# Performance work log

Measured on AMD Instinct MI355X. Metric: run time of the kernel, lower is better.

The kernel has to match this reference:

```python
import jax, jax.numpy as jnp
import numpy as np

N_IN = 1024
N_OUT = 1024
N_SAMPLES = 64
BATCH = 4096
SIGMA_INITIAL = 0.1
MUMAX_INITIAL = 1.0


def setup_inputs() -> dict:
    key = jax.random.key(0)
    ks = jax.random.split(key, 5)
    lsig = jnp.float32(np.log(SIGMA_INITIAL))
    return {
        "x": jax.random.normal(ks[0], (BATCH, N_IN), dtype=jnp.float32),
        "w_mu": jax.random.uniform(ks[1], (N_OUT, N_IN), dtype=jnp.float32,
                                   minval=-MUMAX_INITIAL, maxval=MUMAX_INITIAL),
        "w_lsigma": jnp.full((N_OUT, N_IN), lsig, dtype=jnp.float32),
        "b_mu": jax.random.uniform(ks[2], (N_OUT,), dtype=jnp.float32,
                                   minval=-MUMAX_INITIAL, maxval=MUMAX_INITIAL),
        "b_lsigma": jnp.full((N_OUT,), lsig, dtype=jnp.float32),
        "r1": jax.random.normal(ks[3], (N_SAMPLES, N_OUT, N_IN), dtype=jnp.float32),
        "r2": jax.random.normal(ks[4], (N_SAMPLES, N_OUT), dtype=jnp.float32),
        "N_samples": N_SAMPLES,
    }


def reference(x, w_mu, w_lsigma, b_mu, b_lsigma, r1, r2, N_samples):
    # Reparameterized weight/bias samples: (S, N_out, N_in), (S, N_out)
    w = w_mu + jnp.exp(w_lsigma) * r1
    b = b_mu + jnp.exp(b_lsigma) * r2
    # y[s, b, o] = sum_i x[b, i] * w[s, o, i] + b[s, o]
    y = jnp.einsum('bi,soi->sbo', x, w) + b[:, None, :]
    return y
```

## Files before the change

### kernel.cpp

```cpp
#include <hip/hip_runtime.h>
#include <hip/hip_bf16.h>
#include <hip/hip_fp8.h>
#include <stdint.h>
#include <type_traits>

#define NIN  1024
#define NOUT 1024
#define NB   4096

typedef float f32x4  __attribute__((ext_vector_type(4)));
typedef float f32x16 __attribute__((ext_vector_type(16)));
typedef __bf16 bf16x8 __attribute__((ext_vector_type(8)));
typedef int   i32x4 __attribute__((ext_vector_type(4)));
typedef int   i32x8 __attribute__((ext_vector_type(8)));

typedef const __attribute__((address_space(1))) unsigned int* gp1_t;
typedef __attribute__((address_space(3))) unsigned int* lp3_t;

__device__ __forceinline__ void gload16(const void* g, void* l) {
    __builtin_amdgcn_global_load_lds((gp1_t)g, (lp3_t)l, 16, 0, 0);
}

__device__ __forceinline__ unsigned short f2bf(float f) {
    __bf16 h = (__bf16)f;
    return __builtin_bit_cast(unsigned short, h);
}

__device__ __forceinline__ unsigned int pk4_fp8(float a, float b, float c, float d) {
#if __has_builtin(__builtin_amdgcn_cvt_pk_fp8_f32)
    int p = __builtin_amdgcn_cvt_pk_fp8_f32(a, b, 0, false);
    p = __builtin_amdgcn_cvt_pk_fp8_f32(c, d, p, true);
    return (unsigned int)p;
#else
    __hip_fp8_e4m3 qa(a), qb(b), qc(c), qd(d);
    return (unsigned int)qa.__x | ((unsigned int)qb.__x << 8) |
           ((unsigned int)qc.__x << 16) | ((unsigned int)qd.__x << 24);
#endif
}

#define BAR   __builtin_amdgcn_s_barrier()
#define LGK0  do { asm volatile("s_waitcnt lgkmcnt(0)" ::: "memory"); __builtin_amdgcn_sched_barrier(0); } while (0)
#define VMW8  do { asm volatile("s_waitcnt vmcnt(8)"  ::: "memory"); __builtin_amdgcn_sched_barrier(0); } while (0)
#define VMW2  do { asm volatile("s_waitcnt vmcnt(2)"  ::: "memory"); __builtin_amdgcn_sched_barrier(0); } while (0)
#define VMW0  do { asm volatile("s_waitcnt vmcnt(0)"  ::: "memory"); __builtin_amdgcn_sched_barrier(0); } while (0)

__global__ void cvt_x_both(const float* __restrict__ x, unsigned short* __restrict__ xb,
                           unsigned int* __restrict__ xf8) {
    int i = blockIdx.x * blockDim.x + threadIdx.x;
    f32x4 v = reinterpret_cast<const f32x4*>(x)[i];
    ushort4 o;
    o.x = f2bf(v.x); o.y = f2bf(v.y); o.z = f2bf(v.z); o.w = f2bf(v.w);
    reinterpret_cast<ushort4*>(xb)[i] = o;
    xf8[i] = pk4_fp8(v.x, v.y, v.z, v.w);
}

__global__ void cvt_x_kernel(const float* __restrict__ x, unsigned short* __restrict__ xb) {
    int i = blockIdx.x * blockDim.x + threadIdx.x;
    f32x4 v = reinterpret_cast<const f32x4*>(x)[i];
    ushort4 o;
    o.x = f2bf(v.x); o.y = f2bf(v.y); o.z = f2bf(v.z); o.w = f2bf(v.w);
    reinterpret_cast<ushort4*>(xb)[i] = o;
}

__global__ void cvt_r1_fp8(const float* __restrict__ wls, const float* __restrict__ r1,
                           unsigned int* __restrict__ rf8, int s0) {
    int idx = blockIdx.x * blockDim.x + threadIdx.x;
    int i4 = idx & 262143;
    int c  = idx >> 18;
    f32x4 ls = reinterpret_cast<const f32x4*>(wls)[i4];
    const f32x4* rp = reinterpret_cast<const f32x4*>(r1 + ((size_t)(s0 + c) << 20));
    f32x4 r = __builtin_nontemporal_load(rp + i4);
    rf8[idx] = pk4_fp8(__expf(ls.x) * r.x, __expf(ls.y) * r.y,
                       __expf(ls.z) * r.z, __expf(ls.w) * r.w);
}

__global__ void bias_kernel(const float* __restrict__ bmu, const float* __restrict__ bls,
                            const float* __restrict__ r2, float* __restrict__ bias, int total) {
    int i = blockIdx.x * blockDim.x + threadIdx.x;
    if (i < total) {
        int o = i & (NOUT - 1);
        bias[i] = bmu[o] + __expf(bls[o]) * r2[i];
    }
}

__launch_bounds__(512, 2)
__global__ void gemm256(const unsigned short* __restrict__ xb,
                        const unsigned short* __restrict__ wb,
                        unsigned short* __restrict__ yb, int nwg) {
    __shared__ __align__(16) char smem[131072];
    const int tid = threadIdx.x;
    const int l   = tid & 63;
    const int w   = tid >> 6;
    const int wr  = w >> 2, wc = w & 3;

    const int b   = blockIdx.x;
    const int q8  = nwg >> 3;
    const int g   = (b & 7) * q8 + (b >> 3);
    const int mi  = g & 15;
    const int ni  = g >> 4;
    const int m0  = mi * 256;
    const int n0  = ni * 256;

    const int srow = l >> 3;
    const int scol = ((l & 7) ^ srow) * 8;
    const size_t slane = (size_t)srow * NIN + scol;

    const int rowp  = (l & 15) * 128;
    const int colp0 = ((l >> 4) ^ (l & 7)) << 4;

    f32x4 acc[8][4] = {};
    bf16x8 aF[4][2], b0F[2][2], b1F[2][2];

    const unsigned short* xbase = xb + (size_t)m0 * NIN;
    const unsigned short* wbase = wb + (size_t)n0 * NIN;

    auto STAGE = [&](int buf, int kt, int q) {
        const int R = (q & 3) * 64 + w * 8;
        const unsigned short* src = ((q < 4) ? xbase : wbase)
                                    + (size_t)R * NIN + kt * 64 + slane;
        char* dst = smem + buf * 65536 + ((q >= 4) ? 32768 : 0) + R * 128;
        gload16(src, dst);
    };
    auto LDA = [&](int buf, int mh) {
        const char* base = smem + buf * 65536 + (wr * 128 + mh * 64) * 128 + rowp;
        #pragma unroll
        for (int mb = 0; mb < 4; ++mb) {
            aF[mb][0] = *(const bf16x8*)(base + mb * 2048 + colp0);
            aF[mb][1] = *(const bf16x8*)(base + mb * 2048 + (colp0 ^ 64));
        }
    };
    auto LDB = [&](bf16x8 (&bF)[2][2], int buf, int nh) {
        const char* base = smem + buf * 65536 + 32768 + (wc * 64 + nh * 32) * 128 + rowp;
        #pragma unroll
        for (int nb = 0; nb < 2; ++nb) {
            bF[nb][0] = *(const bf16x8*)(base + nb * 2048 + colp0);
            bF[nb][1] = *(const bf16x8*)(base + nb * 2048 + (colp0 ^ 64));
        }
    };
    auto MM = [&](auto MHc, auto NHc, bf16x8 (&bF)[2][2]) {
        constexpr int MH = decltype(MHc)::value;
        constexpr int NH = decltype(NHc)::value;
        __builtin_amdgcn_s_setprio(1);
        #pragma unroll
        for (int mb = 0; mb < 4; ++mb)
            #pragma unroll
            for (int nb = 0; nb < 2; ++nb)
                #pragma unroll
                for (int kk = 0; kk < 2; ++kk)
                    acc[MH * 4 + mb][NH * 2 + nb] = __builtin_amdgcn_mfma_f32_16x16x32_bf16(
                        aF[mb][kk], bF[nb][kk], acc[MH * 4 + mb][NH * 2 + nb], 0, 0, 0);
        __builtin_amdgcn_s_setprio(0);
    };

    auto C0 = std::integral_constant<int, 0>{};
    auto C1 = std::integral_constant<int, 1>{};

    auto ITER = [&](auto LASTc, int t1, int t2, int t3) {
        constexpr bool LAST = decltype(LASTc)::value;
        LDA(0, 0); LDB(b0F, 0, 0);
        STAGE(1, t1, 2); STAGE(1, t1, 3);
        BAR; LGK0; MM(C0, C0, b0F); BAR;
        LDB(b1F, 0, 1);
        STAGE(1, t1, 4); STAGE(1, t1, 5);
        BAR; LGK0; MM(C0, C1, b1F); BAR;
        LDA(0, 1);
        STAGE(1, t1, 6); STAGE(1, t1, 7);
        BAR; LGK0; MM(C1, C1, b1F); BAR;
        if constexpr (!LAST) { STAGE(0, t2, 0); STAGE(0, t2, 1); }
        BAR; MM(C1, C0, b0F);
        if constexpr (LAST) { VMW0; } else { VMW2; }
        BAR;
        LDA(1, 0); LDB(b0F, 1, 0);
        if constexpr (!LAST) { STAGE(0, t2, 2); STAGE(0, t2, 3); }
        BAR; LGK0; MM(C0, C0, b0F); BAR;
        LDB(b1F, 1, 1);
        if constexpr (!LAST) { STAGE(0, t2, 4); STAGE(0, t2, 5); }
        BAR; LGK0; MM(C0, C1, b1F); BAR;
        LDA(1, 1);
        if constexpr (!LAST) { STAGE(0, t2, 6); STAGE(0, t2, 7); }
        BAR; LGK0; MM(C1, C1, b1F); BAR;
        if constexpr (!LAST) {
            STAGE(1, t3, 0); STAGE(1, t3, 1);
            BAR; MM(C1, C0, b0F); VMW2; BAR;
        } else {
            MM(C1, C0, b0F);
        }
    };

    #pragma unroll
    for (int q = 0; q < 8; ++q) STAGE(0, 0, q);
    STAGE(1, 1, 0); STAGE(1, 1, 1);
    VMW2; BAR;

    #pragma unroll 1
    for (int i = 0; i < 7; ++i)
        ITER(std::false_type{}, 2 * i + 1, 2 * i + 2, 2 * i + 3);
    ITER(std::true_type{}, 15, 16, 17);

    const int oc = n0 + wc * 64 + (l & 15);
    #pragma unroll
    for (int mb = 0; mb < 8; ++mb) {
        #pragma unroll
        for (int i2 = 0; i2 < 4; ++i2) {
            int row = m0 + wr * 128 + mb * 16 + (l >> 4) * 4 + i2;
            unsigned short* rp = yb + (size_t)row * NOUT + oc;
            #pragma unroll
            for (int nb = 0; nb < 4; ++nb)
                rp[nb * 16] = f2bf(acc[mb][nb][i2]);
        }
    }
}

__launch_bounds__(512, 2)
__global__ void gemm256mx(const unsigned char* __restrict__ xf8,
                          const unsigned char* __restrict__ rf8,
                          const unsigned short* __restrict__ y0b,
                          const float* __restrict__ bias,
                          float* __restrict__ out, int s0, int nwg) {
    __shared__ __align__(16) char smem[131072];
    const int tid = threadIdx.x;
    const int l   = tid & 63;
    const int w   = tid >> 6;
    const int wr  = w >> 2, wc = w & 3;

    const int b   = blockIdx.x;
    const int q8  = nwg >> 3;
    const int g   = (b & 7) * q8 + (b >> 3);
    const int nni = nwg >> 4;
    const int mi  = g / nni;
    const int ni  = g - mi * nni;
    const int m0  = mi * 256;
    const int n0  = ni * 256;

    const int srow  = l >> 3;
    const int scolb = ((l & 7) ^ srow) * 16;
    const size_t slane = (size_t)srow * NIN + scolb;

    const int arow = l & 31;
    const int swz  = l & 7;
    const int kgrp = (l >> 5) * 2;

    f32x16 acc[4][2] = {};
    i32x8 aF[2][2], b0F[2], b1F[2];

    const unsigned char* xbase = xf8 + (size_t)m0 * NIN;
    const unsigned char* rbase = rf8 + (size_t)n0 * NIN;

    auto STAGE = [&](int buf, int kt, int q) {
        const int R = (q & 3) * 64 + w * 8;
        const unsigned char* src = ((q < 4) ? xbase : rbase)
                                   + (size_t)R * NIN + kt * 128 + slane;
        char* dst = smem + buf * 65536 + ((q >= 4) ? 32768 : 0) + R * 128;
        gload16(src, dst);
    };
    auto STAGE8 = [&](int buf, int kt) {
        #pragma unroll
        for (int q = 0; q < 8; ++q) STAGE(buf, kt, q);
    };

    auto LDA = [&](int buf, int mh) {
        const char* base = smem + buf * 65536 + (wr * 128 + mh * 64 + arow) * 128;
        #pragma unroll
        for (int mb = 0; mb < 2; ++mb) {
            const char* rb = base + mb * 4096;
            #pragma unroll
            for (int ks = 0; ks < 2; ++ks) {
                int c = ks * 4 + kgrp;
                i32x4 lo = *(const i32x4*)(rb + ((c ^ swz) * 16));
                i32x4 hi = *(const i32x4*)(rb + (((c + 1) ^ swz) * 16));
                aF[mb][ks] = __builtin_shufflevector(lo, hi, 0, 1, 2, 3, 4, 5, 6, 7);
            }
        }
    };
    auto LDB = [&](i32x8 (&bF)[2], int buf, int nh) {
        const char* base = smem + buf * 65536 + 32768 + (wc * 64 + nh * 32 + arow) * 128;
        #pragma unroll
        for (int ks = 0; ks < 2; ++ks) {
            int c = ks * 4 + kgrp;
            i32x4 lo = *(const i32x4*)(base + ((c ^ swz) * 16));
            i32x4 hi = *(const i32x4*)(base + (((c + 1) ^ swz) * 16));
            bF[ks] = __builtin_shufflevector(lo, hi, 0, 1, 2, 3, 4, 5, 6, 7);
        }
    };

    auto MM = [&](auto MHc, auto NHc, i32x8 (&bF)[2]) {
        constexpr int MH = decltype(MHc)::value;
        constexpr int NH = decltype(NHc)::value;
        __builtin_amdgcn_s_setprio(1);
        #pragma unroll
        for (int mb = 0; mb < 2; ++mb)
            #pragma unroll
            for (int ks = 0; ks < 2; ++ks)
                acc[MH * 2 + mb][NH] = __builtin_amdgcn_mfma_scale_f32_32x32x64_f8f6f4(
                    aF[mb][ks], bF[ks], acc[MH * 2 + mb][NH],
                    0, 0, 0, 127, 0, 127);
        __builtin_amdgcn_s_setprio(0);
    };

    auto C0 = std::integral_constant<int, 0>{};
    auto C1 = std::integral_constant<int, 1>{};

    auto ITER = [&](auto LASTc, int t2, int t3) {
        constexpr bool LAST = decltype(LASTc)::value;
        LDA(0, 0); LDB(b0F, 0, 0);
        BAR; LGK0; MM(C0, C0, b0F); BAR;
        LDB(b1F, 0, 1);
        BAR; LGK0; MM(C0, C1, b1F); BAR;
        LDA(0, 1);
        BAR; LGK0; MM(C1, C1, b1F); BAR;
        if constexpr (!LAST) STAGE8(0, t2);
        BAR; MM(C1, C0, b0F);
        if constexpr (LAST) { VMW0; } else { VMW8; }
        BAR;
        LDA(1, 0); LDB(b0F, 1, 0);
        BAR; LGK0; MM(C0, C0, b0F); BAR;
        LDB(b1F, 1, 1);
        BAR; LGK0; MM(C0, C1, b1F); BAR;
        LDA(1, 1);
        BAR; LGK0; MM(C1, C1, b1F); BAR;
        if constexpr (!LAST) {
            STAGE8(1, t3);
            BAR; MM(C1, C0, b0F); VMW8; BAR;
        } else {
            MM(C1, C0, b0F);
        }
    };

    STAGE8(0, 0);
    STAGE8(1, 1);
    VMW8; BAR;

    #pragma unroll 1
    for (int i = 0; i < 3; ++i)
        ITER(std::false_type{}, 2 * i + 2, 2 * i + 3);
    ITER(std::true_type{}, 8, 9);

    const int s   = s0 + (n0 >> 10);
    const int n0c = n0 & 1023;
    float* outp = out + (size_t)s * NB * NOUT;
    float* lds_f = (float*)smem;
    const f32x4 bvv = *(const f32x4*)(bias + (size_t)s * NOUT + n0c + l * 4);

    #pragma unroll
    for (int c = 0; c < 4; ++c) {
        if (wr == (c >> 1)) {
            #pragma unroll
            for (int mbh = 0; mbh < 2; ++mbh) {
                const int mb = (c & 1) * 2 + mbh;
                #pragma unroll
                for (int nb = 0; nb < 2; ++nb) {
                    const int col = wc * 64 + nb * 32 + (l & 31);
                    #pragma unroll
                    for (int r = 0; r < 16; ++r) {
                        int rl = mbh * 32 + 4 * (l >> 5) + (r & 3) + 8 * (r >> 2);
                        lds_f[rl * 256 + col] = acc[mb][nb][r];
                    }
                }
            }
        }
        LGK0; BAR;
        #pragma unroll
        for (int k = 0; k < 8; ++k) {
            const int rl  = k * 8 + w;
            const int row = m0 + c * 64 + rl;
            f32x4 v  = *(const f32x4*)(lds_f + (rl * 64 + l) * 4);
            ushort4 yu = *(const ushort4*)(y0b + (size_t)row * NOUT + n0c + l * 4);
            f32x4 yv;
            yv.x = __builtin_bit_cast(float, (unsigned int)yu.x << 16);
            yv.y = __builtin_bit_cast(float, (unsigned int)yu.y << 16);
            yv.z = __builtin_bit_cast(float, (unsigned int)yu.z << 16);
            yv.w = __builtin_bit_cast(float, (unsigned int)yu.w << 16);
            f32x4 o  = v + yv + bvv;
            __builtin_nontemporal_store(o, (f32x4*)(outp + (size_t)row * NOUT + n0c + l * 4));
        }
        BAR;
    }
}

__global__ void fused_fallback(const float* __restrict__ x, const float* __restrict__ wmu,
                               const float* __restrict__ wls, const float* __restrict__ r1,
                               const float* __restrict__ bmu, const float* __restrict__ bls,
                               const float* __restrict__ r2, float* __restrict__ out) {
    __shared__ float Xs[16][64];
    __shared__ float Ws[16][64];
    int b0 = blockIdx.x * 16, o0 = blockIdx.y * 16, s = blockIdx.z;
    int tb = threadIdx.x >> 4, to = threadIdx.x & 15;
    float acc = 0.f;
    for (int k0 = 0; k0 < NIN; k0 += 64) {
        __syncthreads();
        #pragma unroll
        for (int j = 0; j < 4; ++j) {
            int e = j * 256 + threadIdx.x;
            int r = e >> 6, cc = e & 63;
            Xs[r][cc] = x[(size_t)(b0 + r) * NIN + k0 + cc];
            size_t wi = (size_t)(o0 + r) * NIN + k0 + cc;
            Ws[r][cc] = wmu[wi] + __expf(wls[wi]) * r1[(size_t)s * NIN * NOUT + wi];
        }
        __syncthreads();
        for (int k = 0; k < 64; ++k) acc += Xs[tb][k] * Ws[to][k];
    }
    int o = o0 + to;
    out[((size_t)s * NB + b0 + tb) * NOUT + o] = acc + bmu[o] + __expf(bls[o]) * r2[s * NOUT + o];
}

extern "C" void kernel_launch(void* const* d_in, const int* in_sizes, int n_in,
                              void* d_out, int out_size, void* d_ws, size_t ws_size,
                              hipStream_t stream) {
    const float* x   = (const float*)d_in[0];
    const float* wmu = (const float*)d_in[1];
    const float* wls = (const float*)d_in[2];
    const float* bmu = (const float*)d_in[3];
    const float* bls = (const float*)d_in[4];
    const float* r1  = (const float*)d_in[5];
    const float* r2  = (const float*)d_in[6];
    const int S = in_sizes[6] / NOUT;
    float* out = (float*)d_out;

    const size_t xb_b   = (size_t)NB * NIN * 2;
    const size_t xf8_b  = (size_t)NB * NIN;
    const size_t wmub_b = (size_t)NOUT * NIN * 2;
    const size_t y0_b   = (size_t)NB * NOUT * 2;
    const size_t bias_b = (size_t)S * NOUT * 4;
    const size_t per_s  = (size_t)NOUT * NIN;
    const size_t base_b = xb_b + xf8_b + wmub_b + y0_b + bias_b;

    if (ws_size < base_b + per_s) {
        dim3 gg(NB / 16, NOUT / 16, S);
        fused_fallback<<<gg, 256, 0, stream>>>(x, wmu, wls, r1, bmu, bls, r2, out);
        return;
    }

    char* ws = (char*)d_ws;
    unsigned short* xb   = (unsigned short*)ws;
    unsigned char*  xf8  = (unsigned char*)(ws + xb_b);
    unsigned short* wmub = (unsigned short*)(ws + xb_b + xf8_b);
    unsigned short* y0b  = (unsigned short*)(ws + xb_b + xf8_b + wmub_b);
    float*          bias = (float*)(ws + xb_b + xf8_b + wmub_b + y0_b);
    unsigned char*  rf8  = (unsigned char*)(ws + base_b);

    int SC = (int)((ws_size - base_b) / per_s);
    if (SC > S) SC = S;

    cvt_x_both<<<NB * NIN / 1024, 256, 0, stream>>>(x, xb, (unsigned int*)xf8);
    cvt_x_kernel<<<NOUT * NIN / 1024, 256, 0, stream>>>(wmu, wmub);
    bias_kernel<<<(S * NOUT + 255) / 256, 256, 0, stream>>>(bmu, bls, r2, bias, S * NOUT);

    gemm256<<<64, 512, 0, stream>>>(xb, wmub, y0b, 64);

    for (int s0 = 0; s0 < S; s0 += SC) {
        int sc = (S - s0 < SC) ? (S - s0) : SC;
        cvt_r1_fp8<<<sc * (NOUT * NIN / 1024), 256, 0, stream>>>(wls, r1, (unsigned int*)rf8, s0);
        int nwg = 64 * sc;
        gemm256mx<<<nwg, 512, 0, stream>>>(xf8, rf8, y0b, bias, out, s0, nwg);
    }
}
```

Before: 525.7 us.

## Fuse mean GEMM, r1 fp8 conversion and bias into one prep kernel

Merges the bf16 mean-weight GEMM, the r1-to-fp8 noise conversion and the bias computation into a single launch, with blocks split by role. The 64 GEMM blocks run concurrently with 448 grid-stride conversion blocks and 16 bias blocks, so the small GEMM no longer leaves most CUs idle and fewer launches are needed. The tradeoff is that the conversion blocks reserve the GEMM's 128KB shared memory allocation, which limits occupancy for the bandwidth-bound conversion work.

```diff
diff --git a/kernel.cpp b/kernel.cpp
--- a/kernel.cpp
+++ b/kernel.cpp
@@ -7,6 +7,7 @@
 #define NIN  1024
 #define NOUT 1024
 #define NB   4096
+#define NCVT 448
 
 typedef float f32x4  __attribute__((ext_vector_type(4)));
 typedef float f32x16 __attribute__((ext_vector_type(16)));
@@ -62,40 +63,52 @@
     reinterpret_cast<ushort4*>(xb)[i] = o;
 }
 
-__global__ void cvt_r1_fp8(const float* __restrict__ wls, const float* __restrict__ r1,
-                           unsigned int* __restrict__ rf8, int s0) {
-    int idx = blockIdx.x * blockDim.x + threadIdx.x;
-    int i4 = idx & 262143;
-    int c  = idx >> 18;
-    f32x4 ls = reinterpret_cast<const f32x4*>(wls)[i4];
-    const f32x4* rp = reinterpret_cast<const f32x4*>(r1 + ((size_t)(s0 + c) << 20));
-    f32x4 r = __builtin_nontemporal_load(rp + i4);
-    rf8[idx] = pk4_fp8(__expf(ls.x) * r.x, __expf(ls.y) * r.y,
-                       __expf(ls.z) * r.z, __expf(ls.w) * r.w);
-}
-
-__global__ void bias_kernel(const float* __restrict__ bmu, const float* __restrict__ bls,
-                            const float* __restrict__ r2, float* __restrict__ bias, int total) {
-    int i = blockIdx.x * blockDim.x + threadIdx.x;
-    if (i < total) {
-        int o = i & (NOUT - 1);
-        bias[i] = bmu[o] + __expf(bls[o]) * r2[i];
-    }
-}
-
+template <bool DO_Y0>
 __launch_bounds__(512, 2)
-__global__ void gemm256(const unsigned short* __restrict__ xb,
-                        const unsigned short* __restrict__ wb,
-                        unsigned short* __restrict__ yb, int nwg) {
+__global__ void fused_prep(const unsigned short* __restrict__ xb,
+                           const unsigned short* __restrict__ wb,
+                           unsigned short* __restrict__ yb,
+                           const float* __restrict__ wls,
+                           const float* __restrict__ r1,
+                           unsigned int* __restrict__ rf8,
+                           const float* __restrict__ bmu,
+                           const float* __restrict__ bls,
+                           const float* __restrict__ r2,
+                           float* __restrict__ bias,
+                           int s0, int sc, int stot) {
     __shared__ __align__(16) char smem[131072];
+    const int bid = blockIdx.x;
+
+    if (!DO_Y0 || bid >= 64) {
+        const int cbid = DO_Y0 ? (bid - 64) : bid;
+        if (cbid < NCVT) {
+            const unsigned int U = (unsigned int)sc << 18;
+            for (unsigned int u = cbid * 512u + threadIdx.x; u < U; u += NCVT * 512u) {
+                unsigned int i4 = u & 262143u;
+                unsigned int c  = u >> 18;
+                f32x4 ls = reinterpret_cast<const f32x4*>(wls)[i4];
+                const f32x4* rp = reinterpret_cast<const f32x4*>(r1 + ((size_t)(s0 + c) << 20));
+                f32x4 r = __builtin_nontemporal_load(rp + i4);
+                rf8[u] = pk4_fp8(__expf(ls.x) * r.x, __expf(ls.y) * r.y,
+                                 __expf(ls.z) * r.z, __expf(ls.w) * r.w);
+            }
+        } else if (DO_Y0) {
+            const int total = stot * NOUT;
+            for (int i = (cbid - NCVT) * 512 + threadIdx.x; i < total; i += 16 * 512) {
+                int o = i & (NOUT - 1);
+                bias[i] = bmu[o] + __expf(bls[o]) * r2[i];
+            }
+        }
+        return;
+    }
+
     const int tid = threadIdx.x;
     const int l   = tid & 63;
     const int w   = tid >> 6;
     const int wr  = w >> 2, wc = w & 3;
 
-    const int b   = blockIdx.x;
-    const int q8  = nwg >> 3;
-    const int g   = (b & 7) * q8 + (b >> 3);
+    const int b   = bid;
+    const int g   = (b & 7) * 8 + (b >> 3);
     const int mi  = g & 15;
     const int ni  = g >> 4;
     const int m0  = mi * 256;
@@ -443,13 +456,18 @@
 
     cvt_x_both<<<NB * NIN / 1024, 256, 0, stream>>>(x, xb, (unsigned int*)xf8);
     cvt_x_kernel<<<NOUT * NIN / 1024, 256, 0, stream>>>(wmu, wmub);
-    bias_kernel<<<(S * NOUT + 255) / 256, 256, 0, stream>>>(bmu, bls, r2, bias, S * NOUT);
-
-    gemm256<<<64, 512, 0, stream>>>(xb, wmub, y0b, 64);
-
+
+    bool first = true;
     for (int s0 = 0; s0 < S; s0 += SC) {
         int sc = (S - s0 < SC) ? (S - s0) : SC;
-        cvt_r1_fp8<<<sc * (NOUT * NIN / 1024), 256, 0, stream>>>(wls, r1, (unsigned int*)rf8, s0);
+        if (first) {
+            fused_prep<true><<<64 + NCVT + 16, 512, 0, stream>>>(
+                xb, wmub, y0b, wls, r1, (unsigned int*)rf8, bmu, bls, r2, bias, s0, sc, S);
+            first = false;
+        } else {
+            fused_prep<false><<<NCVT, 512, 0, stream>>>(
+                xb, wmub, y0b, wls, r1, (unsigned int*)rf8, bmu, bls, r2, bias, s0, sc, S);
+        }
         int nwg = 64 * sc;
         gemm256mx<<<nwg, 512, 0, stream>>>(xf8, rf8, y0b, bias, out, s0, nwg);
     }
```

Result: slower. 540.4 us (+2.8%).
